# Optimization experiments

Hardware: AMD Instinct MI355X
Metric: run time of the kernel (lower is better)

The kernel has to match this reference:

```python
import jax, jax.numpy as jnp
import numpy as np

B, H, W = 2, 112, 112
GRID = 128            # vertex grid side -> nver = GRID*GRID
NVER = GRID * GRID    # 16384
NTRI = 8192
NEG_DEPTH = -999999.0  # matches torch 'deep_depth_buffer' fill


def setup_inputs() -> dict:
    key = jax.random.key(0)
    k1, k2, k3, k4, k5 = jax.random.split(key, 5)
    # Vertices laid out on a jittered 2D grid spanning the image (face-mesh-like
    # locality so triangle bounding boxes are small, as in a real PRNet mesh).
    ii, jj = np.meshgrid(np.arange(GRID), np.arange(GRID), indexing='ij')
    base_x = jnp.asarray(jj.ravel() * ((W - 1) / (GRID - 1)), jnp.float32)
    base_y = jnp.asarray(ii.ravel() * ((H - 1) / (GRID - 1)), jnp.float32)
    jit_xy = jax.random.normal(k1, (2, NVER), jnp.float32) * 0.3
    x = jnp.broadcast_to(base_x + jit_xy[0], (B, NVER))
    y = jnp.broadcast_to(base_y + jit_xy[1], (B, NVER))
    z = jax.random.normal(k2, (B, NVER), jnp.float32)
    vertices = jnp.stack([x, y, z], axis=1)            # [B, 3, NVER]
    colors = jax.random.uniform(k3, (B, 3, NVER), jnp.float32)
    # Triangles connect adjacent grid vertices (cell corner, right, below).
    ri = jax.random.randint(k4, (NTRI,), 0, GRID - 1)
    rj = jax.random.randint(k5, (NTRI,), 0, GRID - 1)
    t0 = ri * GRID + rj
    triangles = jnp.stack([t0, t0 + 1, t0 + GRID]).astype(jnp.int32)  # [3, NTRI]
    return {"vertices": vertices, "colors": colors, "triangles": triangles,
            "h": H, "w": W}


def reference(vertices, colors, triangles, h, w):
    # vertices: [B,3,NVER], colors: [B,3,NVER], triangles: [3,NTRI]
    # Per-triangle flat depth and flat color (mean of the 3 corner values).
    tri_depth = vertices[:, 2, :][:, triangles].mean(axis=1)   # [B, NTRI]
    tri_tex = colors[:, :, triangles].mean(axis=2)             # [B, 3, NTRI]
    # Integer pixel bounding box per triangle, clipped to the image.
    tx = vertices[:, 0, :][:, triangles]                        # [B, 3, NTRI]
    ty = vertices[:, 1, :][:, triangles]
    umin = jnp.maximum(jnp.ceil(tx.min(axis=1)), 0.0).astype(jnp.int32)
    umax = jnp.minimum(jnp.floor(tx.max(axis=1)), w - 1).astype(jnp.int32)
    vmin = jnp.maximum(jnp.ceil(ty.min(axis=1)), 0.0).astype(jnp.int32)
    vmax = jnp.minimum(jnp.floor(ty.max(axis=1)), h - 1).astype(jnp.int32)
    valid = (umin <= umax) & (vmin <= vmax)                     # [B, NTRI]
    # Dense per-pixel coverage test against every triangle bbox (same structure
    # the torch code materializes), then argmax z-buffer over triangles.
    ys = jnp.arange(h)[:, None, None]                           # [H,1,1]
    xs = jnp.arange(w)[None, :, None]                           # [1,W,1]
    covered = (valid[:, None, None, :]
               & (ys >= vmin[:, None, None, :]) & (ys <= vmax[:, None, None, :])
               & (xs >= umin[:, None, None, :]) & (xs <= umax[:, None, None, :]))  # [B,H,W,NTRI]
    depth = jnp.where(covered, tri_depth[:, None, None, :], jnp.float32(NEG_DEPTH))
    best = jnp.argmax(depth, axis=-1)                           # [B,H,W] nearest triangle
    any_cov = covered.any(axis=-1)                              # [B,H,W]
    color = jax.vmap(lambda tex, idx: tex[:, idx])(tri_tex, best)  # [B,3,H,W]
    image = jnp.where(any_cov[:, None, :, :], color, 0.0)
    face_mask = any_cov[:, None, :, :].astype(jnp.float32)      # [B,1,H,W]
    return face_mask, image
```

## Files before the change

kernel.cpp:

```cpp
#include <hip/hip_runtime.h>

#define GRID_SIDE 128
#define NVER (GRID_SIDE * GRID_SIDE)
#define NTRI 8192
#define BATCH 2
#define IMG_H 112
#define IMG_W 112
#define HW (IMG_H * IMG_W)

__device__ __forceinline__ unsigned int float_to_ordered(float f) {
    unsigned int u = __float_as_uint(f);
    return (u & 0x80000000u) ? ~u : (u | 0x80000000u);
}

__global__ void zero_keys_kernel(unsigned long long* __restrict__ keys) {
    int tid = blockIdx.x * blockDim.x + threadIdx.x;
    if (tid < BATCH * HW) keys[tid] = 0ull;
}

__global__ void prep_scatter_kernel(const float* __restrict__ vertices,
                                    const float* __restrict__ colors,
                                    const int*   __restrict__ triangles,
                                    unsigned long long* __restrict__ keys,
                                    float* __restrict__ tri_tex)
{
    int tid = blockIdx.x * blockDim.x + threadIdx.x;
    if (tid >= BATCH * NTRI) return;

    int b   = tid / NTRI;
    int tri = tid - b * NTRI;

    int i0 = triangles[tri];
    int i1 = triangles[NTRI + tri];
    int i2 = triangles[2 * NTRI + tri];

    const float* vb = vertices + (size_t)b * 3 * NVER;
    float x0 = vb[i0],            x1 = vb[i1],            x2 = vb[i2];
    float y0 = vb[NVER + i0],     y1 = vb[NVER + i1],     y2 = vb[NVER + i2];
    float z0 = vb[2 * NVER + i0], z1 = vb[2 * NVER + i1], z2 = vb[2 * NVER + i2];

    float depth = (z0 + z1 + z2) * (1.0f / 3.0f);

    const float* cb = colors + (size_t)b * 3 * NVER;
    #pragma unroll
    for (int ch = 0; ch < 3; ++ch) {
        float cc = (cb[ch * NVER + i0] + cb[ch * NVER + i1] + cb[ch * NVER + i2])
                 * (1.0f / 3.0f);
        tri_tex[(size_t)b * 3 * NTRI + ch * NTRI + tri] = cc;
    }

    float xmin = fminf(fminf(x0, x1), x2), xmax = fmaxf(fmaxf(x0, x1), x2);
    float ymin = fminf(fminf(y0, y1), y2), ymax = fmaxf(fmaxf(y0, y1), y2);

    int umin = (int)fmaxf(ceilf(xmin), 0.0f);
    int umax = (int)fminf(floorf(xmax), (float)(IMG_W - 1));
    int vmin = (int)fmaxf(ceilf(ymin), 0.0f);
    int vmax = (int)fminf(floorf(ymax), (float)(IMG_H - 1));
    if (umin > umax || vmin > vmax) return;

    unsigned long long key =
        ((unsigned long long)float_to_ordered(depth) << 32) |
        (unsigned long long)(unsigned int)(~tri);

    unsigned long long* kb = keys + (size_t)b * HW;
    for (int v = vmin; v <= vmax; ++v)
        for (int u = umin; u <= umax; ++u)
            atomicMax(kb + v * IMG_W + u, key);
}

__global__ void resolve_kernel(const unsigned long long* __restrict__ keys,
                               const float* __restrict__ tri_tex,
                               float* __restrict__ out)
{
    int tid = blockIdx.x * blockDim.x + threadIdx.x;
    if (tid >= BATCH * HW) return;

    int b   = tid / HW;
    int pix = tid - b * HW;

    unsigned long long key = keys[tid];

    float* mask  = out;
    float* image = out + BATCH * HW;

    if (key == 0ull) {
        mask[tid] = 0.0f;
        #pragma unroll
        for (int ch = 0; ch < 3; ++ch)
            image[(size_t)b * 3 * HW + ch * HW + pix] = 0.0f;
    } else {
        int tri = (int)(~(unsigned int)(key & 0xFFFFFFFFull));
        mask[tid] = 1.0f;
        #pragma unroll
        for (int ch = 0; ch < 3; ++ch)
            image[(size_t)b * 3 * HW + ch * HW + pix] =
                tri_tex[(size_t)b * 3 * NTRI + ch * NTRI + tri];
    }
}

extern "C" void kernel_launch(void* const* d_in, const int* in_sizes, int n_in,
                              void* d_out, int out_size, void* d_ws, size_t ws_size,
                              hipStream_t stream) {
    const float* vertices  = (const float*)d_in[0];
    const float* colors    = (const float*)d_in[1];
    const int*   triangles = (const int*)d_in[2];

    float* out = (float*)d_out;

    char* ws = (char*)d_ws;
    unsigned long long* keys = (unsigned long long*)(ws);
    float* tri_tex           = (float*)(ws + 200704);

    const int BLK = 256;
    zero_keys_kernel<<<(BATCH * HW + BLK - 1) / BLK, BLK, 0, stream>>>(keys);
    prep_scatter_kernel<<<(BATCH * NTRI + BLK - 1) / BLK, BLK, 0, stream>>>(
        vertices, colors, triangles, keys, tri_tex);
    resolve_kernel<<<(BATCH * HW + BLK - 1) / BLK, BLK, 0, stream>>>(
        keys, tri_tex, out);
}
```

Before: 69.01 us.

## Fuse rasterization into one kernel with LDS z-buffer per image strip

Replaces the three kernels (zero, scatter, resolve) with a single kernel in which each block owns one horizontal strip of one batch image. It keeps the 64-bit depth/index keys in shared memory and uses LDS atomics instead of global atomics. Per-triangle colours are recomputed only for winning pixels during resolve, which removes the tri_tex workspace. Only 8 blocks run, so most of the GPU sits idle. Every block also re-reads all triangles to cull them against its strip.

```diff
diff --git a/kernel.cpp b/kernel.cpp
--- a/kernel.cpp
+++ b/kernel.cpp
@@ -7,94 +7,89 @@
 #define IMG_H 112
 #define IMG_W 112
 #define HW (IMG_H * IMG_W)
+#define STRIPS 4
+#define STRIP_ROWS (IMG_H / STRIPS)
+#define STRIP_PIX (STRIP_ROWS * IMG_W)
+#define NTHREADS 1024
 
 __device__ __forceinline__ unsigned int float_to_ordered(float f) {
     unsigned int u = __float_as_uint(f);
     return (u & 0x80000000u) ? ~u : (u | 0x80000000u);
 }
 
-__global__ void zero_keys_kernel(unsigned long long* __restrict__ keys) {
-    int tid = blockIdx.x * blockDim.x + threadIdx.x;
-    if (tid < BATCH * HW) keys[tid] = 0ull;
-}
+__global__ __launch_bounds__(NTHREADS)
+void raster_fused_kernel(const float* __restrict__ vertices,
+                         const float* __restrict__ colors,
+                         const int*   __restrict__ triangles,
+                         float* __restrict__ out)
+{
+    __shared__ unsigned long long lkeys[STRIP_PIX];
 
-__global__ void prep_scatter_kernel(const float* __restrict__ vertices,
-                                    const float* __restrict__ colors,
-                                    const int*   __restrict__ triangles,
-                                    unsigned long long* __restrict__ keys,
-                                    float* __restrict__ tri_tex)
-{
-    int tid = blockIdx.x * blockDim.x + threadIdx.x;
-    if (tid >= BATCH * NTRI) return;
+    const int bx    = blockIdx.x;
+    const int b     = bx / STRIPS;
+    const int strip = bx - b * STRIPS;
+    const int row0  = strip * STRIP_ROWS;
+    const int tid   = threadIdx.x;
 
-    int b   = tid / NTRI;
-    int tri = tid - b * NTRI;
-
-    int i0 = triangles[tri];
-    int i1 = triangles[NTRI + tri];
-    int i2 = triangles[2 * NTRI + tri];
+    for (int i = tid; i < STRIP_PIX; i += NTHREADS) lkeys[i] = 0ull;
+    __syncthreads();
 
     const float* vb = vertices + (size_t)b * 3 * NVER;
-    float x0 = vb[i0],            x1 = vb[i1],            x2 = vb[i2];
-    float y0 = vb[NVER + i0],     y1 = vb[NVER + i1],     y2 = vb[NVER + i2];
-    float z0 = vb[2 * NVER + i0], z1 = vb[2 * NVER + i1], z2 = vb[2 * NVER + i2];
+    for (int t = tid; t < NTRI; t += NTHREADS) {
+        int i0 = triangles[t];
+        int i1 = triangles[NTRI + t];
+        int i2 = triangles[2 * NTRI + t];
 
-    float depth = (z0 + z1 + z2) * (1.0f / 3.0f);
+        float y0 = vb[NVER + i0], y1 = vb[NVER + i1], y2 = vb[NVER + i2];
+        float ymin = fminf(fminf(y0, y1), y2), ymax = fmaxf(fmaxf(y0, y1), y2);
+        int vmin = (int)fmaxf(ceilf(ymin), 0.0f);
+        int vmax = (int)fminf(floorf(ymax), (float)(IMG_H - 1));
+        int v0 = max(vmin, row0), v1 = min(vmax, row0 + STRIP_ROWS - 1);
+        if (v0 > v1) continue;
 
-    const float* cb = colors + (size_t)b * 3 * NVER;
-    #pragma unroll
-    for (int ch = 0; ch < 3; ++ch) {
-        float cc = (cb[ch * NVER + i0] + cb[ch * NVER + i1] + cb[ch * NVER + i2])
-                 * (1.0f / 3.0f);
-        tri_tex[(size_t)b * 3 * NTRI + ch * NTRI + tri] = cc;
+        float x0 = vb[i0], x1 = vb[i1], x2 = vb[i2];
+        float xmin = fminf(fminf(x0, x1), x2), xmax = fmaxf(fmaxf(x0, x1), x2);
+        int umin = (int)fmaxf(ceilf(xmin), 0.0f);
+        int umax = (int)fminf(floorf(xmax), (float)(IMG_W - 1));
+        if (umin > umax) continue;
+
+        float z0 = vb[2 * NVER + i0], z1 = vb[2 * NVER + i1], z2 = vb[2 * NVER + i2];
+        float depth = (z0 + z1 + z2) * (1.0f / 3.0f);
+
+        unsigned long long key =
+            ((unsigned long long)float_to_ordered(depth) << 32) |
+            (unsigned long long)(unsigned int)(~t);
+
+        for (int v = v0; v <= v1; ++v)
+            for (int u = umin; u <= umax; ++u)
+                atomicMax(&lkeys[(v - row0) * IMG_W + u], key);
     }
+    __syncthreads();
 
-    float xmin = fminf(fminf(x0, x1), x2), xmax = fmaxf(fmaxf(x0, x1), x2);
-    float ymin = fminf(fminf(y0, y1), y2), ymax = fmaxf(fmaxf(y0, y1), y2);
-
-    int umin = (int)fmaxf(ceilf(xmin), 0.0f);
-    int umax = (int)fminf(floorf(xmax), (float)(IMG_W - 1));
-    int vmin = (int)fmaxf(ceilf(ymin), 0.0f);
-    int vmax = (int)fminf(floorf(ymax), (float)(IMG_H - 1));
-    if (umin > umax || vmin > vmax) return;
-
-    unsigned long long key =
-        ((unsigned long long)float_to_ordered(depth) << 32) |
-        (unsigned long long)(unsigned int)(~tri);
-
-    unsigned long long* kb = keys + (size_t)b * HW;
-    for (int v = vmin; v <= vmax; ++v)
-        for (int u = umin; u <= umax; ++u)
-            atomicMax(kb + v * IMG_W + u, key);
-}
-
-__global__ void resolve_kernel(const unsigned long long* __restrict__ keys,
-                               const float* __restrict__ tri_tex,
-                               float* __restrict__ out)
-{
-    int tid = blockIdx.x * blockDim.x + threadIdx.x;
-    if (tid >= BATCH * HW) return;
-
-    int b   = tid / HW;
-    int pix = tid - b * HW;
-
-    unsigned long long key = keys[tid];
-
-    float* mask  = out;
-    float* image = out + BATCH * HW;
-
-    if (key == 0ull) {
-        mask[tid] = 0.0f;
-        #pragma unroll
-        for (int ch = 0; ch < 3; ++ch)
-            image[(size_t)b * 3 * HW + ch * HW + pix] = 0.0f;
-    } else {
-        int tri = (int)(~(unsigned int)(key & 0xFFFFFFFFull));
-        mask[tid] = 1.0f;
-        #pragma unroll
-        for (int ch = 0; ch < 3; ++ch)
-            image[(size_t)b * 3 * HW + ch * HW + pix] =
-                tri_tex[(size_t)b * 3 * NTRI + ch * NTRI + tri];
+    const float* cb    = colors + (size_t)b * 3 * NVER;
+    float*       mask  = out + (size_t)b * HW;
+    float*       image = out + (size_t)BATCH * HW + (size_t)b * 3 * HW;
+    for (int i = tid; i < STRIP_PIX; i += NTHREADS) {
+        int pix = row0 * IMG_W + i;
+        unsigned long long key = lkeys[i];
+        if (key == 0ull) {
+            mask[pix] = 0.0f;
+            image[pix] = 0.0f;
+            image[HW + pix] = 0.0f;
+            image[2 * HW + pix] = 0.0f;
+        } else {
+            int t  = (int)(~(unsigned int)(key & 0xFFFFFFFFull));
+            int i0 = triangles[t];
+            int i1 = triangles[NTRI + t];
+            int i2 = triangles[2 * NTRI + t];
+            mask[pix] = 1.0f;
+            #pragma unroll
+            for (int ch = 0; ch < 3; ++ch) {
+                float cc = (cb[ch * NVER + i0] + cb[ch * NVER + i1] + cb[ch * NVER + i2])
+                         * (1.0f / 3.0f);
+                image[ch * HW + pix] = cc;
+            }
+        }
     }
 }
 
@@ -104,17 +99,8 @@
     const float* vertices  = (const float*)d_in[0];
     const float* colors    = (const float*)d_in[1];
     const int*   triangles = (const int*)d_in[2];
-
     float* out = (float*)d_out;
 
-    char* ws = (char*)d_ws;
-    unsigned long long* keys = (unsigned long long*)(ws);
-    float* tri_tex           = (float*)(ws + 200704);
-
-    const int BLK = 256;
-    zero_keys_kernel<<<(BATCH * HW + BLK - 1) / BLK, BLK, 0, stream>>>(keys);
-    prep_scatter_kernel<<<(BATCH * NTRI + BLK - 1) / BLK, BLK, 0, stream>>>(
-        vertices, colors, triangles, keys, tri_tex);
-    resolve_kernel<<<(BATCH * HW + BLK - 1) / BLK, BLK, 0, stream>>>(
-        keys, tri_tex, out);
+    raster_fused_kernel<<<BATCH * STRIPS, NTHREADS, 0, stream>>>(
+        vertices, colors, triangles, out);
 }
```

Result: slower. 86.82 us (+25.8%).
